# Optimization experiments

Measured on AMD Instinct MI355X. Metric: run time of the kernel, lower is better.

## Reference

```python
import jax, jax.numpy as jnp
import numpy as np
from math import ceil

RATIO = 0.5
NUM_GRAPHS = 512
NODES_PER_GRAPH = 1024
N = NUM_GRAPHS * NODES_PER_GRAPH
C = 64
E = 16 * N


def setup_inputs() -> dict:
    key = jax.random.key(0)
    k1, k2 = jax.random.split(key)
    x = jax.random.normal(k1, (N, C), dtype=jnp.float32)
    edge_index = jax.random.randint(k2, (2, E), 0, N, dtype=jnp.int64)
    batch = jnp.repeat(jnp.arange(NUM_GRAPHS, dtype=jnp.int64), NODES_PER_GRAPH)
    return {"x": x, "edge_index": edge_index, "batch": batch,
            "num_graphs": NUM_GRAPHS, "max_num_nodes": NODES_PER_GRAPH}


def reference(x, edge_index, batch, num_graphs, max_num_nodes):
    n = max_num_nodes
    k_sel = ceil(n * RATIO)
    num_nodes = x.shape[0]
    # per-graph: sorted random subset of k_sel local node ids, offset by graph block
    keys = jax.random.split(jax.random.key(42), num_graphs)
    local = jax.vmap(lambda k: jnp.sort(jax.random.permutation(k, n)[:k_sel]))(keys)  # [B, k_sel]
    offsets = jnp.arange(num_graphs, dtype=local.dtype)[:, None] * n
    perm = (local + offsets).reshape(-1)  # [B*k_sel] global node ids, sorted within each graph

    x_sel = x[perm]
    batch_sel = batch[perm]

    # filter_adj: relabel kept nodes 0..K-1, drop edges touching removed nodes
    idx_dtype = edge_index.dtype
    mask = jnp.full((num_nodes,), -1, dtype=idx_dtype)
    mask = mask.at[perm].set(jnp.arange(perm.shape[0], dtype=idx_dtype))
    row = mask[edge_index[0]]
    col = mask[edge_index[1]]
    keep = (row >= 0) & (col >= 0)
    # fixed-shape variant of the dynamic filter: dropped edges marked -1
    new_edge_index = jnp.where(keep[None, :], jnp.stack([row, col]), -1)
    return (x_sel, new_edge_index, batch_sel, perm)
```

## Files before the change

kernel.cpp:

```cpp
#include <hip/hip_runtime.h>

#define NUM_GRAPHS 512
#define NPG        1024
#define KSEL       512
#define NNODES     (NUM_GRAPHS * NPG)
#define CFEAT      64
#define NEDGE      (16 * NNODES)
#define NWORDS     (NUM_GRAPHS * 32)

typedef int   int4v   __attribute__((ext_vector_type(4)));
typedef float float4v __attribute__((ext_vector_type(4)));

__device__ __forceinline__ unsigned rotl32(unsigned v, int d) {
  return (v << d) | (v >> (32 - d));
}

__device__ __forceinline__ void tf2x32(unsigned k0, unsigned k1,
                                       unsigned x0, unsigned x1,
                                       unsigned& o0, unsigned& o1) {
  unsigned ks2 = k0 ^ k1 ^ 0x1BD11BDAu;
  x0 += k0; x1 += k1;
  x0 += x1; x1 = rotl32(x1, 13); x1 ^= x0;
  x0 += x1; x1 = rotl32(x1, 15); x1 ^= x0;
  x0 += x1; x1 = rotl32(x1, 26); x1 ^= x0;
  x0 += x1; x1 = rotl32(x1, 6);  x1 ^= x0;
  x0 += k1; x1 += ks2 + 1u;
  x0 += x1; x1 = rotl32(x1, 17); x1 ^= x0;
  x0 += x1; x1 = rotl32(x1, 29); x1 ^= x0;
  x0 += x1; x1 = rotl32(x1, 16); x1 ^= x0;
  x0 += x1; x1 = rotl32(x1, 24); x1 ^= x0;
  x0 += ks2; x1 += k0 + 2u;
  x0 += x1; x1 = rotl32(x1, 13); x1 ^= x0;
  x0 += x1; x1 = rotl32(x1, 15); x1 ^= x0;
  x0 += x1; x1 = rotl32(x1, 26); x1 ^= x0;
  x0 += x1; x1 = rotl32(x1, 6);  x1 ^= x0;
  x0 += k0; x1 += k1 + 3u;
  x0 += x1; x1 = rotl32(x1, 17); x1 ^= x0;
  x0 += x1; x1 = rotl32(x1, 29); x1 ^= x0;
  x0 += x1; x1 = rotl32(x1, 16); x1 ^= x0;
  x0 += x1; x1 = rotl32(x1, 24); x1 ^= x0;
  x0 += k1; x1 += ks2 + 4u;
  x0 += x1; x1 = rotl32(x1, 13); x1 ^= x0;
  x0 += x1; x1 = rotl32(x1, 15); x1 ^= x0;
  x0 += x1; x1 = rotl32(x1, 26); x1 ^= x0;
  x0 += x1; x1 = rotl32(x1, 6);  x1 ^= x0;
  x0 += ks2; x1 += k0 + 5u;
  o0 = x0; o1 = x1;
}

__global__ __launch_bounds__(512) void select_kernel(
    float* __restrict__ out_b, float* __restrict__ out_p,
    unsigned long long* __restrict__ tab, unsigned short* __restrict__ ids_ws) {
  __shared__ unsigned long long skeys[NPG];
  __shared__ int flags[NPG];
  __shared__ short ids[KSEL];
  __shared__ int ssum[512];

  const int g = blockIdx.x;
  const int tid = threadIdx.x;

  unsigned kg0, kg1, sk0, sk1;
  tf2x32(0u, 42u, 0u, (unsigned)g, kg0, kg1);
  tf2x32(kg0, kg1, 0u, 1u, sk0, sk1);

  for (int i = tid; i < NPG; i += 512) {
    unsigned b1, b2;
    tf2x32(sk0, sk1, 0u, (unsigned)i, b1, b2);
    unsigned key = b1 ^ b2;
    skeys[i] = ((unsigned long long)key << 32) | (unsigned)i;
    flags[i] = 0;
  }
  __syncthreads();

  for (int k = 2; k <= NPG; k <<= 1) {
    for (int j = k >> 1; j > 0; j >>= 1) {
      for (int i = tid; i < NPG; i += 512) {
        int ixj = i ^ j;
        if (ixj > i) {
          unsigned long long a = skeys[i], b = skeys[ixj];
          bool up = ((i & k) == 0);
          if ((a > b) == up) { skeys[i] = b; skeys[ixj] = a; }
        }
      }
      __syncthreads();
    }
  }

  if (tid < KSEL) flags[(int)(skeys[tid] & (unsigned long long)(NPG - 1))] = 1;
  __syncthreads();

  int i2 = tid * 2;
  int f0 = flags[i2], f1 = flags[i2 + 1];
  int local = f0 + f1;
  ssum[tid] = local;
  __syncthreads();
  for (int off = 1; off < 512; off <<= 1) {
    int v = (tid >= off) ? ssum[tid - off] : 0;
    __syncthreads();
    ssum[tid] += v;
    __syncthreads();
  }
  int pos = ssum[tid] - local;

  {
    int i = i2;
    int node = g * NPG + i;
    if (f0) {
      ids[pos] = (short)i;
      out_b[g * KSEL + pos] = (float)g;
      out_p[g * KSEL + pos] = (float)node;
      pos++;
    }
    if (f1) {
      ids[pos] = (short)(i + 1);
      out_b[g * KSEL + pos] = (float)g;
      out_p[g * KSEL + pos] = (float)(node + 1);
    }
  }

  if (tid < 32) {
    unsigned w = 0;
#pragma unroll
    for (int j = 0; j < 32; ++j) w |= ((unsigned)(flags[tid * 32 + j] & 1)) << j;
    unsigned base = (tid == 0) ? 0u : (unsigned)ssum[tid * 16 - 1];
    tab[g * 32 + tid] = (unsigned long long)w |
                        ((unsigned long long)base << 32);
  }
  __syncthreads();

  if (tid < KSEL) ids_ws[g * KSEL + tid] = (unsigned short)ids[tid];
}

__global__ __launch_bounds__(1024) void fused_kernel(
    const float* __restrict__ x, const int* __restrict__ ei,
    const unsigned long long* __restrict__ tab,
    const unsigned short* __restrict__ ids_ws,
    float* __restrict__ out_x, float* __restrict__ out_e) {
  __shared__ unsigned long long ltab[NWORDS];
  __shared__ unsigned short lids[1024];

  const int tid = threadIdx.x;
  const int blk = blockIdx.x;

#pragma unroll
  for (int k = 0; k < NWORDS / 1024; ++k) {
    ltab[k * 1024 + tid] = tab[k * 1024 + tid];
  }
  {
    const int row0 = blk * 1024;
    if (tid < 512) {
      ((unsigned*)lids)[tid] = ((const unsigned*)(ids_ws + row0))[tid];
    }
  }
  __syncthreads();

  {
    const float4v* xs = (const float4v*)x;
    float4v* xd = (float4v*)out_x;
    const int row0 = blk * 1024;
#pragma unroll
    for (int k = 0; k < 16; ++k) {
      int t = k * 1024 + tid;
      int r = t >> 4;
      int c = t & 15;
      int row = row0 + r;
      int g = row >> 9;
      int id = lids[r];
      float4v v = __builtin_nontemporal_load(
          &xs[((size_t)g * NPG + id) * 16 + c]);
      __builtin_nontemporal_store(v, &xd[(size_t)row * 16 + c]);
    }
  }

#pragma unroll
  for (int k = 0; k < 4; ++k) {
    const int base = (((k * 256 + blk) * 1024) + tid) * 8;
    int4v s0 = __builtin_nontemporal_load((const int4v*)(ei + base));
    int4v s1 = __builtin_nontemporal_load((const int4v*)(ei + base + 4));
    int4v d0 = __builtin_nontemporal_load((const int4v*)(ei + (size_t)NEDGE + base));
    int4v d1 = __builtin_nontemporal_load((const int4v*)(ei + (size_t)NEDGE + base + 4));

    int src[8] = {s0.x, s0.y, s0.z, s0.w, s1.x, s1.y, s1.z, s1.w};
    int dst[8] = {d0.x, d0.y, d0.z, d0.w, d1.x, d1.y, d1.z, d1.w};

    int rrow[8], rcol[8];
#pragma unroll
    for (int j = 0; j < 8; ++j) {
      unsigned long long es = ltab[src[j] >> 5];
      unsigned long long ed = ltab[dst[j] >> 5];
      unsigned ws = (unsigned)es, wd = (unsigned)ed;
      int shs = src[j] & 31, shd = dst[j] & 31;
      bool sels = (ws >> shs) & 1u;
      bool seld = (wd >> shd) & 1u;
      int poss = (int)(es >> 32) + __popc(ws & ((1u << shs) - 1u));
      int posd = (int)(ed >> 32) + __popc(wd & ((1u << shd) - 1u));
      bool keep = sels && seld;
      rrow[j] = keep ? (((src[j] & ~1023) >> 1) + poss) : -1;
      rcol[j] = keep ? (((dst[j] & ~1023) >> 1) + posd) : -1;
    }

    float4v r0 = {(float)rrow[0], (float)rrow[1], (float)rrow[2], (float)rrow[3]};
    float4v r1 = {(float)rrow[4], (float)rrow[5], (float)rrow[6], (float)rrow[7]};
    float4v c0 = {(float)rcol[0], (float)rcol[1], (float)rcol[2], (float)rcol[3]};
    float4v c1 = {(float)rcol[4], (float)rcol[5], (float)rcol[6], (float)rcol[7]};
    __builtin_nontemporal_store(r0, (float4v*)(out_e + base));
    __builtin_nontemporal_store(r1, (float4v*)(out_e + base + 4));
    __builtin_nontemporal_store(c0, (float4v*)(out_e + (size_t)NEDGE + base));
    __builtin_nontemporal_store(c1, (float4v*)(out_e + (size_t)NEDGE + base + 4));
  }
}

extern "C" void kernel_launch(void* const* d_in, const int* in_sizes, int n_in,
                              void* d_out, int out_size, void* d_ws, size_t ws_size,
                              hipStream_t stream) {
  const float* x  = (const float*)d_in[0];
  const int*   ei = (const int*)d_in[1];

  float* out   = (float*)d_out;
  float* out_x = out;
  float* out_e = out + (size_t)NUM_GRAPHS * KSEL * CFEAT;
  float* out_b = out_e + 2 * (size_t)NEDGE;
  float* out_p = out_b + (size_t)NUM_GRAPHS * KSEL;

  unsigned long long* tab = (unsigned long long*)d_ws;
  unsigned short* ids_ws = (unsigned short*)((char*)d_ws + NWORDS * 8);

  select_kernel<<<NUM_GRAPHS, 512, 0, stream>>>(out_b, out_p, tab, ids_ws);
  fused_kernel<<<256, 1024, 0, stream>>>(x, ei, tab, ids_ws, out_x, out_e);
}
```

Baseline: 298.8 us.

## Replace bitonic sort with radix-bin selection and move feature gather into select kernel

The full 1024-element bitonic sort per graph is replaced by a top-byte histogram, a prefix scan to find the bin holding the 512th key, and a brute-force rank within that bin to get the threshold key. Nodes whose key is at or below the threshold are flagged. The x-row gather moves from the edge kernel into the select kernel, which drops the ids workspace round trip and lets the gather overlap with selection work across blocks. The cost is shared-memory atomics and a quadratic rank step over a small candidate set.

```diff
diff --git a/kernel.cpp b/kernel.cpp
--- a/kernel.cpp
+++ b/kernel.cpp
@@ -49,12 +49,18 @@
 }
 
 __global__ __launch_bounds__(512) void select_kernel(
+    const float* __restrict__ x, float* __restrict__ out_x,
     float* __restrict__ out_b, float* __restrict__ out_p,
-    unsigned long long* __restrict__ tab, unsigned short* __restrict__ ids_ws) {
-  __shared__ unsigned long long skeys[NPG];
+    unsigned long long* __restrict__ tab) {
   __shared__ int flags[NPG];
   __shared__ short ids[KSEL];
   __shared__ int ssum[512];
+  __shared__ int bins[256];
+  __shared__ int binsum[256];
+  __shared__ unsigned long long cand[NPG];
+  __shared__ int ccnt;
+  __shared__ int sB, sR;
+  __shared__ unsigned long long sT;
 
   const int g = blockIdx.x;
   const int tid = threadIdx.x;
@@ -63,30 +69,68 @@
   tf2x32(0u, 42u, 0u, (unsigned)g, kg0, kg1);
   tf2x32(kg0, kg1, 0u, 1u, sk0, sk1);
 
-  for (int i = tid; i < NPG; i += 512) {
+  if (tid < 256) bins[tid] = 0;
+  if (tid == 0) ccnt = 0;
+
+  unsigned long long myk[2];
+#pragma unroll
+  for (int e = 0; e < 2; ++e) {
+    int i = tid + e * 512;
     unsigned b1, b2;
     tf2x32(sk0, sk1, 0u, (unsigned)i, b1, b2);
     unsigned key = b1 ^ b2;
-    skeys[i] = ((unsigned long long)key << 32) | (unsigned)i;
-    flags[i] = 0;
-  }
-  __syncthreads();
-
-  for (int k = 2; k <= NPG; k <<= 1) {
-    for (int j = k >> 1; j > 0; j >>= 1) {
-      for (int i = tid; i < NPG; i += 512) {
-        int ixj = i ^ j;
-        if (ixj > i) {
-          unsigned long long a = skeys[i], b = skeys[ixj];
-          bool up = ((i & k) == 0);
-          if ((a > b) == up) { skeys[i] = b; skeys[ixj] = a; }
-        }
-      }
-      __syncthreads();
-    }
-  }
-
-  if (tid < KSEL) flags[(int)(skeys[tid] & (unsigned long long)(NPG - 1))] = 1;
+    myk[e] = ((unsigned long long)key << 32) | (unsigned)i;
+  }
+  __syncthreads();
+
+#pragma unroll
+  for (int e = 0; e < 2; ++e)
+    atomicAdd(&bins[(int)(myk[e] >> 56)], 1);
+  __syncthreads();
+
+  if (tid < 256) binsum[tid] = bins[tid];
+  __syncthreads();
+  for (int off = 1; off < 256; off <<= 1) {
+    int v = 0;
+    if (tid < 256 && tid >= off) v = binsum[tid - off];
+    __syncthreads();
+    if (tid < 256) binsum[tid] += v;
+    __syncthreads();
+  }
+  if (tid < 256) {
+    int incl = binsum[tid];
+    int excl = incl - bins[tid];
+    if (excl < KSEL && KSEL <= incl) { sB = tid; sR = KSEL - excl; }
+  }
+  __syncthreads();
+  const int bstar = sB;
+  const int r = sR;
+
+#pragma unroll
+  for (int e = 0; e < 2; ++e) {
+    if ((int)(myk[e] >> 56) == bstar) {
+      int p = atomicAdd(&ccnt, 1);
+      cand[p] = myk[e];
+    }
+  }
+  __syncthreads();
+  const int cnt = ccnt;
+  if (tid < 64) {
+    for (int c = tid; c < cnt; c += 64) {
+      unsigned long long mine = cand[c];
+      int rank = 0;
+      for (int j = 0; j < cnt; ++j) rank += (cand[j] < mine) ? 1 : 0;
+      if (rank == r - 1) sT = mine;
+    }
+  }
+  __syncthreads();
+  const unsigned long long T = sT;
+
+#pragma unroll
+  for (int e = 0; e < 2; ++e) {
+    int i = tid + e * 512;
+    flags[i] = (myk[e] <= T) ? 1 : 0;
+  }
   __syncthreads();
 
   int i2 = tid * 2;
@@ -128,16 +172,26 @@
   }
   __syncthreads();
 
-  if (tid < KSEL) ids_ws[g * KSEL + tid] = (unsigned short)ids[tid];
-}
-
-__global__ __launch_bounds__(1024) void fused_kernel(
-    const float* __restrict__ x, const int* __restrict__ ei,
+  {
+    const float4v* xs = (const float4v*)x + (size_t)g * (NPG * 16);
+    float4v* xd = (float4v*)out_x + (size_t)g * (KSEL * 16);
+#pragma unroll
+    for (int k = 0; k < 16; ++k) {
+      int t = k * 512 + tid;
+      int rr = t >> 4;
+      int c = t & 15;
+      int id = (int)ids[rr];
+      float4v v = __builtin_nontemporal_load(&xs[id * 16 + c]);
+      __builtin_nontemporal_store(v, &xd[rr * 16 + c]);
+    }
+  }
+}
+
+__global__ __launch_bounds__(1024) void edge_kernel(
+    const int* __restrict__ ei,
     const unsigned long long* __restrict__ tab,
-    const unsigned short* __restrict__ ids_ws,
-    float* __restrict__ out_x, float* __restrict__ out_e) {
+    float* __restrict__ out_e) {
   __shared__ unsigned long long ltab[NWORDS];
-  __shared__ unsigned short lids[1024];
 
   const int tid = threadIdx.x;
   const int blk = blockIdx.x;
@@ -146,31 +200,7 @@
   for (int k = 0; k < NWORDS / 1024; ++k) {
     ltab[k * 1024 + tid] = tab[k * 1024 + tid];
   }
-  {
-    const int row0 = blk * 1024;
-    if (tid < 512) {
-      ((unsigned*)lids)[tid] = ((const unsigned*)(ids_ws + row0))[tid];
-    }
-  }
-  __syncthreads();
-
-  {
-    const float4v* xs = (const float4v*)x;
-    float4v* xd = (float4v*)out_x;
-    const int row0 = blk * 1024;
-#pragma unroll
-    for (int k = 0; k < 16; ++k) {
-      int t = k * 1024 + tid;
-      int r = t >> 4;
-      int c = t & 15;
-      int row = row0 + r;
-      int g = row >> 9;
-      int id = lids[r];
-      float4v v = __builtin_nontemporal_load(
-          &xs[((size_t)g * NPG + id) * 16 + c]);
-      __builtin_nontemporal_store(v, &xd[(size_t)row * 16 + c]);
-    }
-  }
+  __syncthreads();
 
 #pragma unroll
   for (int k = 0; k < 4; ++k) {
@@ -223,8 +253,7 @@
   float* out_p = out_b + (size_t)NUM_GRAPHS * KSEL;
 
   unsigned long long* tab = (unsigned long long*)d_ws;
-  unsigned short* ids_ws = (unsigned short*)((char*)d_ws + NWORDS * 8);
-
-  select_kernel<<<NUM_GRAPHS, 512, 0, stream>>>(out_b, out_p, tab, ids_ws);
-  fused_kernel<<<256, 1024, 0, stream>>>(x, ei, tab, ids_ws, out_x, out_e);
-}
+
+  select_kernel<<<NUM_GRAPHS, 512, 0, stream>>>(x, out_x, out_b, out_p, tab);
+  edge_kernel<<<256, 1024, 0, stream>>>(ei, tab, out_e);
+}
```

Result: faster. 274.3 us (-8.2%).

## Replace bitonic sort with radix-histogram threshold selection in select kernel

Applied to the files above, without the earlier changes.

The full 1024-element bitonic sort per graph is replaced by a 256-bin histogram on the top key byte, a scan to find the bin holding the 512th key, and a rank count among that bin's candidates to get the exact threshold key. Selected nodes are then compacted using wave ballots and popcount prefix sums, which also build the bitmap table directly. This removes the roughly 55 barrier-separated sort passes and the block-wide scan. In exchange it adds shared-memory atomics and a quadratic rank step over the candidates in one bin, which could be slow if many keys share the top byte.

```diff
diff --git a/kernel.cpp b/kernel.cpp
--- a/kernel.cpp
+++ b/kernel.cpp
@@ -48,87 +48,134 @@
   o0 = x0; o1 = x1;
 }
 
-__global__ __launch_bounds__(512) void select_kernel(
+__global__ __launch_bounds__(512) void tab_kernel(
     float* __restrict__ out_b, float* __restrict__ out_p,
-    unsigned long long* __restrict__ tab, unsigned short* __restrict__ ids_ws) {
-  __shared__ unsigned long long skeys[NPG];
-  __shared__ int flags[NPG];
-  __shared__ short ids[KSEL];
-  __shared__ int ssum[512];
+    unsigned long long* __restrict__ tab,
+    unsigned short* __restrict__ ids_ws) {
+  __shared__ int bins[256];
+  __shared__ unsigned long long cand[NPG];
+  __shared__ unsigned long long words64[16];
+  __shared__ int wbase[16];
+  __shared__ int ccnt;
+  __shared__ int sB, sR;
+  __shared__ unsigned long long sT;
 
   const int g = blockIdx.x;
   const int tid = threadIdx.x;
+  const int lane = tid & 63;
+  const int wv = tid >> 6;
 
   unsigned kg0, kg1, sk0, sk1;
   tf2x32(0u, 42u, 0u, (unsigned)g, kg0, kg1);
   tf2x32(kg0, kg1, 0u, 1u, sk0, sk1);
 
-  for (int i = tid; i < NPG; i += 512) {
+  if (tid < 256) bins[tid] = 0;
+  if (tid == 0) ccnt = 0;
+
+  unsigned long long myk[2];
+#pragma unroll
+  for (int e = 0; e < 2; ++e) {
+    int i = e * 512 + tid;
     unsigned b1, b2;
     tf2x32(sk0, sk1, 0u, (unsigned)i, b1, b2);
     unsigned key = b1 ^ b2;
-    skeys[i] = ((unsigned long long)key << 32) | (unsigned)i;
-    flags[i] = 0;
-  }
-  __syncthreads();
-
-  for (int k = 2; k <= NPG; k <<= 1) {
-    for (int j = k >> 1; j > 0; j >>= 1) {
-      for (int i = tid; i < NPG; i += 512) {
-        int ixj = i ^ j;
-        if (ixj > i) {
-          unsigned long long a = skeys[i], b = skeys[ixj];
-          bool up = ((i & k) == 0);
-          if ((a > b) == up) { skeys[i] = b; skeys[ixj] = a; }
-        }
-      }
-      __syncthreads();
-    }
-  }
-
-  if (tid < KSEL) flags[(int)(skeys[tid] & (unsigned long long)(NPG - 1))] = 1;
-  __syncthreads();
-
-  int i2 = tid * 2;
-  int f0 = flags[i2], f1 = flags[i2 + 1];
-  int local = f0 + f1;
-  ssum[tid] = local;
-  __syncthreads();
-  for (int off = 1; off < 512; off <<= 1) {
-    int v = (tid >= off) ? ssum[tid - off] : 0;
-    __syncthreads();
-    ssum[tid] += v;
-    __syncthreads();
-  }
-  int pos = ssum[tid] - local;
-
+    myk[e] = ((unsigned long long)key << 32) | (unsigned)i;
+  }
+  __syncthreads();
+
+#pragma unroll
+  for (int e = 0; e < 2; ++e)
+    atomicAdd(&bins[(int)(myk[e] >> 56)], 1);
+  __syncthreads();
+
+  if (tid < 64) {
+    int b0 = bins[4 * tid], b1 = bins[4 * tid + 1],
+        b2 = bins[4 * tid + 2], b3 = bins[4 * tid + 3];
+    int s = b0 + b1 + b2 + b3;
+    int inc = s;
+#pragma unroll
+    for (int d = 1; d < 64; d <<= 1) {
+      int t = __shfl_up(inc, d, 64);
+      if (tid >= d) inc += t;
+    }
+    int excl = inc - s;
+    int i0 = excl + b0, i1 = i0 + b1, i2 = i1 + b2, i3 = i2 + b3;
+    if (excl < KSEL && KSEL <= i0) { sB = 4 * tid;     sR = KSEL - excl; }
+    if (i0   < KSEL && KSEL <= i1) { sB = 4 * tid + 1; sR = KSEL - i0; }
+    if (i1   < KSEL && KSEL <= i2) { sB = 4 * tid + 2; sR = KSEL - i1; }
+    if (i2   < KSEL && KSEL <= i3) { sB = 4 * tid + 3; sR = KSEL - i2; }
+  }
+  __syncthreads();
+  const int bstar = sB;
+  const int r = sR;
+
+#pragma unroll
+  for (int e = 0; e < 2; ++e) {
+    if ((int)(myk[e] >> 56) == bstar) {
+      int p = atomicAdd(&ccnt, 1);
+      cand[p] = myk[e];
+    }
+  }
+  __syncthreads();
+  const int cnt = ccnt;
+  if (tid < 64) {
+    for (int c = tid; c < cnt; c += 64) {
+      unsigned long long mine = cand[c];
+      int rank = 0;
+      for (int j = 0; j < cnt; ++j) rank += (cand[j] < mine) ? 1 : 0;
+      if (rank == r - 1) sT = mine;
+    }
+  }
+  __syncthreads();
+  const unsigned long long T = sT;
+
+  const bool sel0 = (myk[0] <= T);
+  const bool sel1 = (myk[1] <= T);
   {
-    int i = i2;
-    int node = g * NPG + i;
-    if (f0) {
-      ids[pos] = (short)i;
+    unsigned long long b0 = __ballot(sel0);
+    unsigned long long b1 = __ballot(sel1);
+    if (lane == 0) {
+      words64[wv] = b0;
+      words64[8 + wv] = b1;
+    }
+  }
+  __syncthreads();
+
+  if (tid < 16) {
+    int c = __popcll(words64[tid]);
+    int inc = c;
+#pragma unroll
+    for (int d = 1; d < 16; d <<= 1) {
+      int t = __shfl_up(inc, d, 64);
+      if (tid >= d) inc += t;
+    }
+    wbase[tid] = inc - c;
+  }
+  __syncthreads();
+
+#pragma unroll
+  for (int e = 0; e < 2; ++e) {
+    bool sel = e ? sel1 : sel0;
+    if (sel) {
+      int i = e * 512 + tid;
+      int wi = i >> 6;
+      int l = i & 63;
+      unsigned long long w = words64[wi];
+      int pos = wbase[wi] + __popcll(w & ((1ull << l) - 1ull));
+      ids_ws[g * KSEL + pos] = (unsigned short)i;
       out_b[g * KSEL + pos] = (float)g;
-      out_p[g * KSEL + pos] = (float)node;
-      pos++;
-    }
-    if (f1) {
-      ids[pos] = (short)(i + 1);
-      out_b[g * KSEL + pos] = (float)g;
-      out_p[g * KSEL + pos] = (float)(node + 1);
+      out_p[g * KSEL + pos] = (float)(g * NPG + i);
     }
   }
 
   if (tid < 32) {
-    unsigned w = 0;
-#pragma unroll
-    for (int j = 0; j < 32; ++j) w |= ((unsigned)(flags[tid * 32 + j] & 1)) << j;
-    unsigned base = (tid == 0) ? 0u : (unsigned)ssum[tid * 16 - 1];
-    tab[g * 32 + tid] = (unsigned long long)w |
+    unsigned long long w64 = words64[tid >> 1];
+    unsigned w32 = (unsigned)(w64 >> ((tid & 1) * 32));
+    unsigned base = (unsigned)wbase[tid >> 1] +
+                    ((tid & 1) ? (unsigned)__popc((unsigned)w64) : 0u);
+    tab[g * 32 + tid] = (unsigned long long)w32 |
                         ((unsigned long long)base << 32);
   }
-  __syncthreads();
-
-  if (tid < KSEL) ids_ws[g * KSEL + tid] = (unsigned short)ids[tid];
 }
 
 __global__ __launch_bounds__(1024) void fused_kernel(
@@ -225,6 +272,6 @@
   unsigned long long* tab = (unsigned long long*)d_ws;
   unsigned short* ids_ws = (unsigned short*)((char*)d_ws + NWORDS * 8);
 
-  select_kernel<<<NUM_GRAPHS, 512, 0, stream>>>(out_b, out_p, tab, ids_ws);
+  tab_kernel<<<NUM_GRAPHS, 512, 0, stream>>>(out_b, out_p, tab, ids_ws);
   fused_kernel<<<256, 1024, 0, stream>>>(x, ei, tab, ids_ws, out_x, out_e);
 }
```

Measured after the change: 279.7 us. 1.07x faster.
